# Optimization experiments

Hardware: AMD Instinct MI355X
Metric: run time of the kernel (lower is better)

The kernel has to match this reference:

```python
import jax, jax.numpy as jnp
import numpy as np

B, S, D, H, E = 2, 1024, 1024, 4096, 8


def _xavier(key, shape):
    # matches torch.nn.init.xavier_uniform_ on a 3D tensor: fan_in/out from last two dims
    fan_in, fan_out = shape[-2], shape[-1]
    limit = float(np.sqrt(6.0 / (fan_in + fan_out)))
    return jax.random.uniform(key, shape, jnp.float32, -limit, limit)


def setup_inputs() -> dict:
    key = jax.random.key(0)
    ks = jax.random.split(key, 4)
    x = jax.random.normal(ks[0], (B, S, D), jnp.float32)
    router_w = jax.random.normal(ks[1], (D, E), jnp.float32) * (1.0 / np.sqrt(D))
    router_b = jnp.zeros((E,), jnp.float32)
    fc1_weight = _xavier(ks[2], (E, D, H))
    fc1_bias = jnp.zeros((E, H), jnp.float32)
    fc2_weight = _xavier(ks[3], (E, H, D))
    fc2_bias = jnp.zeros((E, D), jnp.float32)
    return {
        "x": x,
        "router_w": router_w,
        "router_b": router_b,
        "fc1_weight": fc1_weight,
        "fc1_bias": fc1_bias,
        "fc2_weight": fc2_weight,
        "fc2_bias": fc2_bias,
    }


def reference(x, router_w, router_b, fc1_weight, fc1_bias, fc2_weight, fc2_bias):
    b, s, d = x.shape
    x_flat = x.reshape(-1, d)                                  # [T, D]
    logits = x_flat @ router_w + router_b                       # [T, E]
    probs = jax.nn.softmax(logits, axis=-1)                     # [T, E]
    # per-expert FC1 + exact GELU (torch nn.GELU default is erf-based)
    h = jnp.einsum('td,edh->teh', x_flat, fc1_weight) + fc1_bias  # [T, E, H]
    h = jax.nn.gelu(h, approximate=False)
    expert_out = jnp.einsum('teh,ehd->ted', h, fc2_weight) + fc2_bias  # [T, E, D]
    out_flat = jnp.einsum('te,ted->td', probs, expert_out)      # [T, D]
    y = out_flat.reshape(b, s, d)
    router_probs = probs.reshape(b, s, -1)
    return y, router_probs
```

## Files before the change

kernel.cpp:

```cpp
#include <hip/hip_runtime.h>
#include <math.h>


typedef float f32x4 __attribute__((ext_vector_type(4)));
typedef __bf16 bf16x8 __attribute__((ext_vector_type(8)));

#define GLL16(gp, lp)                                                          \
  __builtin_amdgcn_global_load_lds(                                            \
      (const __attribute__((address_space(1))) void*)(gp),                     \
      (__attribute__((address_space(3))) void*)(lp), 16, 0, 0)

__device__ __forceinline__ float gelu_f(float h) {
  return 0.5f * h * (1.f + erff(h * 0.70710678118654752f));
}

__global__ void router_kernel(const float* __restrict__ x,
                              const float* __restrict__ rw,
                              const float* __restrict__ rb,
                              float* __restrict__ P,
                              float* __restrict__ probs_out)
{
  int gid = blockIdx.x * blockDim.x + threadIdx.x;
  int t = gid >> 6;
  int l = gid & 63;
  const float* xr = x + (size_t)t * 1024;
  float a[8];
#pragma unroll
  for (int e = 0; e < 8; ++e) a[e] = 0.f;
  for (int d = l; d < 1024; d += 64) {
    float xv = xr[d];
    f32x4 w0 = *(const f32x4*)(rw + d * 8);
    f32x4 w1 = *(const f32x4*)(rw + d * 8 + 4);
#pragma unroll
    for (int e = 0; e < 4; ++e) a[e] += xv * w0[e];
#pragma unroll
    for (int e = 0; e < 4; ++e) a[4 + e] += xv * w1[e];
  }
#pragma unroll
  for (int off = 32; off > 0; off >>= 1) {
#pragma unroll
    for (int e = 0; e < 8; ++e) a[e] += __shfl_down(a[e], off);
  }
  if (l == 0) {
#pragma unroll
    for (int e = 0; e < 8; ++e) a[e] += rb[e];
    float m = a[0];
#pragma unroll
    for (int e = 1; e < 8; ++e) m = fmaxf(m, a[e]);
    float s = 0.f;
#pragma unroll
    for (int e = 0; e < 8; ++e) { a[e] = __expf(a[e] - m); s += a[e]; }
    float inv = 1.f / s;
#pragma unroll
    for (int e = 0; e < 8; ++e) {
      float p = a[e] * inv;
      if (P) P[t * 8 + e] = p;
      probs_out[t * 8 + e] = p;
    }
  }
}

__global__ void cvt_kernel(const float* __restrict__ src,
                           __bf16* __restrict__ dst)
{
  size_t i = ((size_t)blockIdx.x * 256 + threadIdx.x) * 8;
  f32x4 v0 = *(const f32x4*)(src + i);
  f32x4 v1 = *(const f32x4*)(src + i + 4);
  bf16x8 o;
#pragma unroll
  for (int j = 0; j < 4; ++j) o[j] = (__bf16)v0[j];
#pragma unroll
  for (int j = 0; j < 4; ++j) o[4 + j] = (__bf16)v1[j];
  *(bf16x8*)(dst + i) = o;
}

__global__ void transconv_kernel(const float* __restrict__ src,
                                 __bf16* __restrict__ dst,
                                 int R, int C, int cChunk,
                                 size_t dstLd, size_t zOff)
{
  size_t bs = (size_t)blockIdx.z * (size_t)R * (size_t)C;
  size_t dzo = (size_t)blockIdx.z * zOff;
  int r = blockIdx.x * 256 + threadIdx.x;
  int c0 = blockIdx.y * cChunk;
  const float* s = src + bs + (size_t)r * C;
  for (int c = c0; c < c0 + cChunk; c += 8) {
    f32x4 v0 = *(const f32x4*)(s + c);
    f32x4 v1 = *(const f32x4*)(s + c + 4);
    float vv[8] = {v0[0], v0[1], v0[2], v0[3], v1[0], v1[1], v1[2], v1[3]};
#pragma unroll
    for (int j = 0; j < 8; ++j)
      dst[(size_t)(c + j) * dstLd + dzo + r] = (__bf16)vv[j];
  }
}

__device__ __forceinline__ void mfma_loop(const __bf16* A, const __bf16* B,
                                          int lda, int ldb, int K,
                                          __bf16* As, __bf16* Bs,
                                          f32x4 acc[4][4])
{
  const int tid = threadIdx.x;
  const int w = tid >> 6, l = tid & 63;
  const int rg = l >> 3;
  const int csrc = ((l & 7) ^ rg) << 4;
  const size_t ldaB = (size_t)lda * 2, ldbB = (size_t)ldb * 2;
  const char* Ab = (const char*)A + (size_t)(w * 32 + rg) * ldaB + csrc;
  const char* Bb = (const char*)B + (size_t)(w * 32 + rg) * ldbB + csrc;
  char* AsW = (char*)As + w * 4096;
  char* BsW = (char*)Bs + w * 4096;
  const int wm = w & 1, wn = w >> 1;
  const int m16 = l & 15, quad = l >> 4;
  const int rowA0 = wm * 64 + m16;
  const int rowB0 = wn * 64 + m16;
  const int sw = m16 & 7;

  for (int k0 = 0; k0 < K; k0 += 64) {
    __syncthreads();
    const size_t kB = (size_t)k0 * 2;
#pragma unroll
    for (int i = 0; i < 4; ++i) {
      GLL16(Ab + kB + (size_t)(8 * i) * ldaB, AsW + i * 1024);
      GLL16(Bb + kB + (size_t)(8 * i) * ldbB, BsW + i * 1024);
    }
    __syncthreads();
#pragma unroll
    for (int kk = 0; kk < 2; ++kk) {
      const int pos = ((quad + 4 * kk) ^ sw) << 3;
      bf16x8 af[4], bfr[4];
#pragma unroll
      for (int i = 0; i < 4; ++i)
        af[i] = *(const bf16x8*)(As + (rowA0 + 16 * i) * 64 + pos);
#pragma unroll
      for (int j = 0; j < 4; ++j)
        bfr[j] = *(const bf16x8*)(Bs + (rowB0 + 16 * j) * 64 + pos);
#pragma unroll
      for (int i = 0; i < 4; ++i)
#pragma unroll
        for (int j = 0; j < 4; ++j)
          acc[i][j] = __builtin_amdgcn_mfma_f32_16x16x32_bf16(
              af[i], bfr[j], acc[i][j], 0, 0, 0);
    }
  }
}

__global__ void gemm1_kernel(const __bf16* __restrict__ X,
                             const __bf16* __restrict__ W1T,
                             const float* __restrict__ b1,
                             const float* __restrict__ P,
                             __bf16* __restrict__ Hs,
                             int hs_ld, int e_off, size_t b_zstride)
{
  __shared__ __bf16 As[128 * 64], Bs[128 * 64];
  const int bm = blockIdx.x, bn = blockIdx.y, z = blockIdx.z;
  const int e = z + e_off;
  f32x4 acc[4][4];
  const f32x4 z4 = {0.f, 0.f, 0.f, 0.f};
#pragma unroll
  for (int i = 0; i < 4; ++i)
#pragma unroll
    for (int j = 0; j < 4; ++j) acc[i][j] = z4;

  const __bf16* A = X + (size_t)bm * 128 * 1024;
  const __bf16* B = W1T + (size_t)z * b_zstride + (size_t)bn * 128 * 1024;
  mfma_loop(A, B, 1024, 1024, 1024, As, Bs, acc);

  const int tid = threadIdx.x, w = tid >> 6, l = tid & 63;
  const int wm = w & 1, wn = w >> 1, q = l >> 4, c16 = l & 15;
  const int row0 = bm * 128 + wm * 64 + q * 4;
  const int col0 = bn * 128 + wn * 64 + c16;
  float b1v[4];
#pragma unroll
  for (int j = 0; j < 4; ++j)
    b1v[j] = b1[(size_t)e * 4096 + col0 + j * 16];
  float pv[4][4];
#pragma unroll
  for (int i = 0; i < 4; ++i)
#pragma unroll
    for (int r = 0; r < 4; ++r)
      pv[i][r] = P[(size_t)(row0 + i * 16 + r) * 8 + e];
  const int zcol = (hs_ld == 4096) ? 0 : z * 4096;
#pragma unroll
  for (int i = 0; i < 4; ++i)
#pragma unroll
    for (int j = 0; j < 4; ++j)
#pragma unroll
      for (int r = 0; r < 4; ++r) {
        float h = acc[i][j][r] + b1v[j];
        float o = gelu_f(h) * pv[i][r];
        Hs[(size_t)(row0 + i * 16 + r) * hs_ld + zcol + col0 + j * 16] =
            (__bf16)o;
      }
}

__global__ void gemm2_kernel(const __bf16* __restrict__ Hs,
                             const __bf16* __restrict__ W2T,
                             float* __restrict__ accb,
                             int lda, int ldb, int kz)
{
  __shared__ __bf16 As[128 * 64], Bs[128 * 64];
  const int bm = blockIdx.x, bn = blockIdx.y, z = blockIdx.z;
  f32x4 acc[4][4];
  const f32x4 z4 = {0.f, 0.f, 0.f, 0.f};
#pragma unroll
  for (int i = 0; i < 4; ++i)
#pragma unroll
    for (int j = 0; j < 4; ++j) acc[i][j] = z4;

  const __bf16* A = Hs + (size_t)bm * 128 * lda + (size_t)z * kz;
  const __bf16* B = W2T + (size_t)bn * 128 * ldb + (size_t)z * kz;
  mfma_loop(A, B, lda, ldb, 4096, As, Bs, acc);

  const int tid = threadIdx.x, w = tid >> 6, l = tid & 63;
  const int wm = w & 1, wn = w >> 1, q = l >> 4, c16 = l & 15;
  const int row0 = bm * 128 + wm * 64 + q * 4;
  const int col0 = bn * 128 + wn * 64 + c16;
#pragma unroll
  for (int i = 0; i < 4; ++i)
#pragma unroll
    for (int j = 0; j < 4; ++j)
#pragma unroll
      for (int r = 0; r < 4; ++r)
        unsafeAtomicAdd(
            accb + (size_t)(row0 + i * 16 + r) * 1024 + col0 + j * 16,
            acc[i][j][r]);
}

__global__ void finalize_kernel(const float* __restrict__ accb,
                                const float* __restrict__ P,
                                const float* __restrict__ b2,
                                float* __restrict__ y)
{
  int idx = blockIdx.x * 256 + threadIdx.x;
  int t = idx >> 8;
  int d0 = (idx & 255) << 2;
  f32x4 a = *(const f32x4*)(accb + (size_t)t * 1024 + d0);
#pragma unroll
  for (int e = 0; e < 8; ++e) {
    float p = P[t * 8 + e];
    f32x4 b = *(const f32x4*)(b2 + (size_t)e * 1024 + d0);
#pragma unroll
    for (int c = 0; c < 4; ++c) a[c] += p * b[c];
  }
  *(f32x4*)(y + (size_t)t * 1024 + d0) = a;
}

__global__ __launch_bounds__(256) void fused_naive_kernel(
    const float* __restrict__ x, const float* __restrict__ w1,
    const float* __restrict__ b1, const float* __restrict__ w2,
    const float* __restrict__ b2, const float* __restrict__ probs,
    float* __restrict__ y)
{
  __shared__ float xs[8][1024];
  __shared__ float gs[8][64];
  __shared__ float ps[8];
  const int tid = threadIdx.x;
  const int t0 = blockIdx.x * 8;
  const size_t DH = (size_t)1024 * 4096;
  const int tt = tid >> 5;
  const int d0 = (tid & 31) * 32;
  float acc[32];
#pragma unroll
  for (int i = 0; i < 32; ++i) acc[i] = 0.f;
  {
    const f32x4* xsrc = (const f32x4*)(x + (size_t)t0 * 1024);
    f32x4* xdst = (f32x4*)&xs[0][0];
    for (int i = tid; i < 2048; i += 256) xdst[i] = xsrc[i];
  }
  const int wv = tid >> 6;
  const int hl = tid & 63;
  for (int e = 0; e < 8; ++e) {
    if (tid < 8) ps[tid] = probs[(size_t)(t0 + tid) * 8 + e];
    __syncthreads();
    for (int hc = 0; hc < 4096; hc += 64) {
      float a0 = 0.f, a1 = 0.f;
      const float* w1p = w1 + (size_t)e * DH + hc + hl;
      for (int d = 0; d < 1024; ++d) {
        float wvv = w1p[(size_t)d * 4096];
        a0 += xs[wv * 2 + 0][d] * wvv;
        a1 += xs[wv * 2 + 1][d] * wvv;
      }
      __syncthreads();
      gs[wv * 2 + 0][hl] =
          ps[wv * 2 + 0] * gelu_f(a0 + b1[(size_t)e * 4096 + hc + hl]);
      gs[wv * 2 + 1][hl] =
          ps[wv * 2 + 1] * gelu_f(a1 + b1[(size_t)e * 4096 + hc + hl]);
      __syncthreads();
      const float* w2p = w2 + (size_t)e * DH + (size_t)hc * 1024 + d0;
      for (int hh = 0; hh < 64; ++hh) {
        float g = gs[tt][hh];
#pragma unroll
        for (int jb = 0; jb < 8; ++jb) {
          f32x4 w4 = *(const f32x4*)(w2p + (size_t)hh * 1024 + jb * 4);
#pragma unroll
          for (int j2 = 0; j2 < 4; ++j2) acc[jb * 4 + j2] += g * w4[j2];
        }
      }
    }
#pragma unroll
    for (int j = 0; j < 32; ++j)
      acc[j] += ps[tt] * b2[(size_t)e * 1024 + d0 + j];
    __syncthreads();
  }
  float* yp = y + (size_t)(t0 + tt) * 1024 + d0;
#pragma unroll
  for (int jb = 0; jb < 8; ++jb) {
    f32x4 o = {acc[jb * 4], acc[jb * 4 + 1], acc[jb * 4 + 2], acc[jb * 4 + 3]};
    *(f32x4*)(yp + jb * 4) = o;
  }
}

extern "C" void kernel_launch(void* const* d_in, const int* in_sizes, int n_in,
                              void* d_out, int out_size, void* d_ws,
                              size_t ws_size, hipStream_t stream)
{
  const float* x  = (const float*)d_in[0];
  const float* rw = (const float*)d_in[1];
  const float* rb = (const float*)d_in[2];
  const float* w1 = (const float*)d_in[3];
  const float* b1 = (const float*)d_in[4];
  const float* w2 = (const float*)d_in[5];
  const float* b2 = (const float*)d_in[6];
  float* y = (float*)d_out;
  float* probs_out = y + (size_t)2048 * 1024;

  const size_t DH = (size_t)1024 * 4096;
  const size_t BASE = (64 << 10) + (size_t)2048 * 1024 * 4 +
                      (size_t)2048 * 1024 * 2;
  const size_t TA = BASE + 8 * DH * 2 + (size_t)2048 * 32768 * 2;
  const size_t TB = BASE + DH * 2 + (size_t)2048 * 4096 * 2;

  char* ws = (char*)d_ws;
  float* P = (float*)ws;
  float* accb = (float*)(ws + (64 << 10));
  __bf16* xb = (__bf16*)(ws + (64 << 10) + (size_t)2048 * 1024 * 4);
  char* ws2 = ws + BASE;

  if (ws_size >= TA) {
    router_kernel<<<512, 256, 0, stream>>>(x, rw, rb, P, probs_out);
    hipMemsetAsync(accb, 0, (size_t)2048 * 1024 * 4, stream);
    cvt_kernel<<<1024, 256, 0, stream>>>(x, xb);
    __bf16* WT = (__bf16*)ws2;
    __bf16* Hs = WT + 8 * DH;
    transconv_kernel<<<dim3(4, 64, 8), 256, 0, stream>>>(
        w1, WT, 1024, 4096, 64, 1024, DH);
    gemm1_kernel<<<dim3(16, 32, 8), 256, 0, stream>>>(xb, WT, b1, P, Hs,
                                                      32768, 0, DH);
    transconv_kernel<<<dim3(16, 16, 8), 256, 0, stream>>>(
        w2, WT, 4096, 1024, 64, 32768, 4096);
    gemm2_kernel<<<dim3(16, 8, 8), 256, 0, stream>>>(Hs, WT, accb, 32768,
                                                     32768, 4096);
    finalize_kernel<<<2048, 256, 0, stream>>>(accb, P, b2, y);
  } else if (ws_size >= TB) {
    router_kernel<<<512, 256, 0, stream>>>(x, rw, rb, P, probs_out);
    hipMemsetAsync(accb, 0, (size_t)2048 * 1024 * 4, stream);
    cvt_kernel<<<1024, 256, 0, stream>>>(x, xb);
    __bf16* WT = (__bf16*)ws2;
    __bf16* HsE = WT + DH;
    for (int e = 0; e < 8; ++e) {
      transconv_kernel<<<dim3(4, 64, 1), 256, 0, stream>>>(
          w1 + e * DH, WT, 1024, 4096, 64, 1024, 0);
      gemm1_kernel<<<dim3(16, 32, 1), 256, 0, stream>>>(xb, WT, b1, P, HsE,
                                                        4096, e, 0);
      transconv_kernel<<<dim3(16, 16, 1), 256, 0, stream>>>(
          w2 + e * DH, WT, 4096, 1024, 64, 4096, 0);
      gemm2_kernel<<<dim3(16, 8, 1), 256, 0, stream>>>(HsE, WT, accb, 4096,
                                                       4096, 0);
    }
    finalize_kernel<<<2048, 256, 0, stream>>>(accb, P, b2, y);
  } else {
    router_kernel<<<512, 256, 0, stream>>>(x, rw, rb, (float*)nullptr,
                                           probs_out);
    fused_naive_kernel<<<256, 256, 0, stream>>>(x, w1, b1, w2, b2, probs_out,
                                                y);
  }
}
```

Measured before the change: 712.6 us.

## Use 256x256 tiles with a 4-stage LDS ring and XCD-aware block swizzle

Rewrites the shared MFMA main loop for both expert GEMMs. It now uses 512-thread workgroups computing 256x256 tiles with K-steps of 32 and a 4-deep LDS ring buffer, so global-to-LDS loads run three stages ahead of compute with explicit waitcnt and a single barrier per step. Block IDs are remapped so that neighbouring tiles land on the same XCD for better L2 reuse, and MFMA priority is raised. In exchange it uses 128KB of LDS and many more accumulator registers per workgroup, which limits occupancy. The per-expert fallback path's gemm2 is also split along K across four z slices.

```diff
diff --git a/kernel.cpp b/kernel.cpp
--- a/kernel.cpp
+++ b/kernel.cpp
@@ -94,135 +94,183 @@
   }
 }
 
-__device__ __forceinline__ void mfma_loop(const __bf16* A, const __bf16* B,
-                                          int lda, int ldb, int K,
-                                          __bf16* As, __bf16* Bs,
-                                          f32x4 acc[4][4])
+__device__ __forceinline__ void mfma_loop256(
+    const char* Ab, const char* Bb, size_t ldaB, size_t ldbB, int K,
+    char* lds, f32x4 acc[8][4])
 {
   const int tid = threadIdx.x;
   const int w = tid >> 6, l = tid & 63;
-  const int rg = l >> 3;
-  const int csrc = ((l & 7) ^ rg) << 4;
-  const size_t ldaB = (size_t)lda * 2, ldbB = (size_t)ldb * 2;
-  const char* Ab = (const char*)A + (size_t)(w * 32 + rg) * ldaB + csrc;
-  const char* Bb = (const char*)B + (size_t)(w * 32 + rg) * ldbB + csrc;
-  char* AsW = (char*)As + w * 4096;
-  char* BsW = (char*)Bs + w * 4096;
-  const int wm = w & 1, wn = w >> 1;
-  const int m16 = l & 15, quad = l >> 4;
-  const int rowA0 = wm * 64 + m16;
-  const int rowB0 = wn * 64 + m16;
-  const int sw = m16 & 7;
-
-  for (int k0 = 0; k0 < K; k0 += 64) {
-    __syncthreads();
-    const size_t kB = (size_t)k0 * 2;
-#pragma unroll
-    for (int i = 0; i < 4; ++i) {
-      GLL16(Ab + kB + (size_t)(8 * i) * ldaB, AsW + i * 1024);
-      GLL16(Bb + kB + (size_t)(8 * i) * ldbB, BsW + i * 1024);
-    }
-    __syncthreads();
-#pragma unroll
-    for (int kk = 0; kk < 2; ++kk) {
-      const int pos = ((quad + 4 * kk) ^ sw) << 3;
-      bf16x8 af[4], bfr[4];
-#pragma unroll
-      for (int i = 0; i < 4; ++i)
-        af[i] = *(const bf16x8*)(As + (rowA0 + 16 * i) * 64 + pos);
-#pragma unroll
-      for (int j = 0; j < 4; ++j)
-        bfr[j] = *(const bf16x8*)(Bs + (rowB0 + 16 * j) * 64 + pos);
-#pragma unroll
-      for (int i = 0; i < 4; ++i)
-#pragma unroll
-        for (int j = 0; j < 4; ++j)
-          acc[i][j] = __builtin_amdgcn_mfma_f32_16x16x32_bf16(
-              af[i], bfr[j], acc[i][j], 0, 0, 0);
-    }
-  }
-}
-
-__global__ void gemm1_kernel(const __bf16* __restrict__ X,
-                             const __bf16* __restrict__ W1T,
-                             const float* __restrict__ b1,
-                             const float* __restrict__ P,
-                             __bf16* __restrict__ Hs,
-                             int hs_ld, int e_off, size_t b_zstride)
-{
-  __shared__ __bf16 As[128 * 64], Bs[128 * 64];
-  const int bm = blockIdx.x, bn = blockIdx.y, z = blockIdx.z;
+  const int wm = w >> 2, wn = w & 3;
+  const int m16 = l & 15, q = l >> 4;
+  const int posB = ((q ^ ((m16 >> 1) & 3)) << 4);
+  const int aE = (wm * 128 + m16) * 64 + posB;
+  const int bE = 16384 + (wn * 64 + m16) * 64 + posB;
+  const int sc16 = (((l & 3) ^ ((l >> 3) & 3)) << 4);
+  const size_t sAoff = (size_t)(w * 32 + (l >> 2)) * ldaB + sc16;
+  const size_t sBoff = (size_t)(w * 32 + (l >> 2)) * ldbB + sc16;
+  const int ldst = w * 32 * 64;
+  const int NT = K >> 5;
+
+#define STAGE256(u)                                                            \
+  {                                                                            \
+    char* dA = lds + (((u) & 3) * 32768) + ldst;                               \
+    const char* gA = Ab + sAoff + ((size_t)(u) << 6);                          \
+    GLL16(gA, dA);                                                             \
+    GLL16(gA + 16 * ldaB, dA + 1024);                                          \
+    char* dB = dA + 16384;                                                     \
+    const char* gB = Bb + sBoff + ((size_t)(u) << 6);                          \
+    GLL16(gB, dB);                                                             \
+    GLL16(gB + 16 * ldbB, dB + 1024);                                          \
+  }
+
+#define KFRAGS(T)                                                              \
+    const char* ring = lds + (((T) & 3) * 32768);                              \
+    bf16x8 af[8], bv[4];                                                       \
+    _Pragma("unroll") for (int mi = 0; mi < 8; ++mi)                           \
+        af[mi] = *(const bf16x8*)(ring + aE + mi * 1024);                      \
+    _Pragma("unroll") for (int nj = 0; nj < 4; ++nj)                           \
+        bv[nj] = *(const bf16x8*)(ring + bE + nj * 1024);
+
+#define KMFMA                                                                  \
+    __builtin_amdgcn_sched_barrier(0);                                         \
+    asm volatile("s_waitcnt lgkmcnt(0)" ::: "memory");                         \
+    __builtin_amdgcn_sched_barrier(0);                                         \
+    __builtin_amdgcn_s_setprio(1);                                             \
+    _Pragma("unroll") for (int mi = 0; mi < 8; ++mi)                           \
+      _Pragma("unroll") for (int nj = 0; nj < 4; ++nj)                         \
+        acc[mi][nj] = __builtin_amdgcn_mfma_f32_16x16x32_bf16(                 \
+            af[mi], bv[nj], acc[mi][nj], 0, 0, 0);                             \
+    __builtin_amdgcn_s_setprio(0);                                             \
+    __builtin_amdgcn_sched_barrier(0);
+
+  STAGE256(0);
+  STAGE256(1);
+  STAGE256(2);
+  asm volatile("s_waitcnt vmcnt(8)" ::: "memory");
+  __builtin_amdgcn_s_barrier();
+
+  int t = 0;
+  for (; t < NT - 3; ++t) {
+    KFRAGS(t);
+    STAGE256(t + 3);
+    KMFMA;
+    asm volatile("s_waitcnt vmcnt(8)" ::: "memory");
+    __builtin_amdgcn_s_barrier();
+  }
+  {
+    KFRAGS(t);
+    KMFMA;
+    asm volatile("s_waitcnt vmcnt(0)" ::: "memory");
+    __builtin_amdgcn_s_barrier();
+  }
+  ++t;
+  {
+    KFRAGS(t);
+    KMFMA;
+  }
+  ++t;
+  {
+    KFRAGS(t);
+    KMFMA;
+  }
+#undef STAGE256
+#undef KFRAGS
+#undef KMFMA
+}
+
+__device__ __forceinline__ int xcd_swz(int id, int nwg) {
+  return ((nwg & 7) == 0) ? ((id & 7) * (nwg >> 3) + (id >> 3)) : id;
+}
+
+__global__ __launch_bounds__(512, 2) void gemm1_kernel(
+    const __bf16* __restrict__ X, const __bf16* __restrict__ W1T,
+    const float* __restrict__ b1, const float* __restrict__ P,
+    __bf16* __restrict__ Hs, int hs_ld, int e_off, size_t b_zstride)
+{
+  __shared__ __align__(16) char lds[131072];
+  const int nwg = gridDim.x * gridDim.y * gridDim.z;
+  const int id = blockIdx.x + gridDim.x * (blockIdx.y + gridDim.y * blockIdx.z);
+  const int wg = xcd_swz(id, nwg);
+  const int bm = wg & 7;
+  const int bn = (wg >> 3) % gridDim.y;
+  const int z = wg / (gridDim.y << 3);
   const int e = z + e_off;
-  f32x4 acc[4][4];
+
+  f32x4 acc[8][4];
   const f32x4 z4 = {0.f, 0.f, 0.f, 0.f};
 #pragma unroll
-  for (int i = 0; i < 4; ++i)
+  for (int i = 0; i < 8; ++i)
 #pragma unroll
     for (int j = 0; j < 4; ++j) acc[i][j] = z4;
 
-  const __bf16* A = X + (size_t)bm * 128 * 1024;
-  const __bf16* B = W1T + (size_t)z * b_zstride + (size_t)bn * 128 * 1024;
-  mfma_loop(A, B, 1024, 1024, 1024, As, Bs, acc);
+  const char* A = (const char*)(X + (size_t)bm * 256 * 1024);
+  const char* B = (const char*)(W1T + (size_t)z * b_zstride +
+                                (size_t)bn * 256 * 1024);
+  mfma_loop256(A, B, 2048, 2048, 1024, lds, acc);
 
   const int tid = threadIdx.x, w = tid >> 6, l = tid & 63;
-  const int wm = w & 1, wn = w >> 1, q = l >> 4, c16 = l & 15;
-  const int row0 = bm * 128 + wm * 64 + q * 4;
-  const int col0 = bn * 128 + wn * 64 + c16;
+  const int wm = w >> 2, wn = w & 3, q = l >> 4, m16 = l & 15;
+  const int row0 = bm * 256 + wm * 128 + q * 4;
+  const int colE = bn * 256 + wn * 64 + m16;
+  const int zcol = (hs_ld == 4096) ? 0 : z * 4096;
   float b1v[4];
 #pragma unroll
-  for (int j = 0; j < 4; ++j)
-    b1v[j] = b1[(size_t)e * 4096 + col0 + j * 16];
-  float pv[4][4];
-#pragma unroll
-  for (int i = 0; i < 4; ++i)
+  for (int nj = 0; nj < 4; ++nj)
+    b1v[nj] = b1[(size_t)e * 4096 + colE + nj * 16];
+#pragma unroll
+  for (int mi = 0; mi < 8; ++mi) {
+    float pv[4];
 #pragma unroll
     for (int r = 0; r < 4; ++r)
-      pv[i][r] = P[(size_t)(row0 + i * 16 + r) * 8 + e];
-  const int zcol = (hs_ld == 4096) ? 0 : z * 4096;
-#pragma unroll
-  for (int i = 0; i < 4; ++i)
-#pragma unroll
-    for (int j = 0; j < 4; ++j)
+      pv[r] = P[(size_t)(row0 + mi * 16 + r) * 8 + e];
+#pragma unroll
+    for (int nj = 0; nj < 4; ++nj)
 #pragma unroll
       for (int r = 0; r < 4; ++r) {
-        float h = acc[i][j][r] + b1v[j];
-        float o = gelu_f(h) * pv[i][r];
-        Hs[(size_t)(row0 + i * 16 + r) * hs_ld + zcol + col0 + j * 16] =
+        float h = acc[mi][nj][r] + b1v[nj];
+        float o = gelu_f(h) * pv[r];
+        Hs[(size_t)(row0 + mi * 16 + r) * hs_ld + zcol + colE + nj * 16] =
             (__bf16)o;
       }
-}
-
-__global__ void gemm2_kernel(const __bf16* __restrict__ Hs,
-                             const __bf16* __restrict__ W2T,
-                             float* __restrict__ accb,
-                             int lda, int ldb, int kz)
-{
-  __shared__ __bf16 As[128 * 64], Bs[128 * 64];
-  const int bm = blockIdx.x, bn = blockIdx.y, z = blockIdx.z;
-  f32x4 acc[4][4];
+  }
+}
+
+__global__ __launch_bounds__(512, 2) void gemm2_kernel(
+    const __bf16* __restrict__ Hs, const __bf16* __restrict__ W2T,
+    float* __restrict__ accb, int lda, int ldb, int kz, int Kb)
+{
+  __shared__ __align__(16) char lds[131072];
+  const int nwg = gridDim.x * gridDim.y * gridDim.z;
+  const int id = blockIdx.x + gridDim.x * (blockIdx.y + gridDim.y * blockIdx.z);
+  const int wg = xcd_swz(id, nwg);
+  const int bm = wg & 7;
+  const int bn = (wg >> 3) % gridDim.y;
+  const int z = wg / (gridDim.y << 3);
+
+  f32x4 acc[8][4];
   const f32x4 z4 = {0.f, 0.f, 0.f, 0.f};
 #pragma unroll
-  for (int i = 0; i < 4; ++i)
+  for (int i = 0; i < 8; ++i)
 #pragma unroll
     for (int j = 0; j < 4; ++j) acc[i][j] = z4;
 
-  const __bf16* A = Hs + (size_t)bm * 128 * lda + (size_t)z * kz;
-  const __bf16* B = W2T + (size_t)bn * 128 * ldb + (size_t)z * kz;
-  mfma_loop(A, B, lda, ldb, 4096, As, Bs, acc);
+  const char* A = (const char*)(Hs + (size_t)bm * 256 * lda + (size_t)z * kz);
+  const char* B = (const char*)(W2T + (size_t)bn * 256 * ldb + (size_t)z * kz);
+  mfma_loop256(A, B, (size_t)lda * 2, (size_t)ldb * 2, Kb, lds, acc);
 
   const int tid = threadIdx.x, w = tid >> 6, l = tid & 63;
-  const int wm = w & 1, wn = w >> 1, q = l >> 4, c16 = l & 15;
-  const int row0 = bm * 128 + wm * 64 + q * 4;
-  const int col0 = bn * 128 + wn * 64 + c16;
-#pragma unroll
-  for (int i = 0; i < 4; ++i)
-#pragma unroll
-    for (int j = 0; j < 4; ++j)
+  const int wm = w >> 2, wn = w & 3, q = l >> 4, m16 = l & 15;
+  const int row0 = bm * 256 + wm * 128 + q * 4;
+  const int col0 = bn * 256 + wn * 64 + m16;
+#pragma unroll
+  for (int mi = 0; mi < 8; ++mi)
+#pragma unroll
+    for (int nj = 0; nj < 4; ++nj)
 #pragma unroll
       for (int r = 0; r < 4; ++r)
         unsafeAtomicAdd(
-            accb + (size_t)(row0 + i * 16 + r) * 1024 + col0 + j * 16,
-            acc[i][j][r]);
+            accb + (size_t)(row0 + mi * 16 + r) * 1024 + col0 + nj * 16,
+            acc[mi][nj][r]);
 }
 
 __global__ void finalize_kernel(const float* __restrict__ accb,
@@ -343,12 +391,12 @@
     __bf16* Hs = WT + 8 * DH;
     transconv_kernel<<<dim3(4, 64, 8), 256, 0, stream>>>(
         w1, WT, 1024, 4096, 64, 1024, DH);
-    gemm1_kernel<<<dim3(16, 32, 8), 256, 0, stream>>>(xb, WT, b1, P, Hs,
-                                                      32768, 0, DH);
+    gemm1_kernel<<<dim3(8, 16, 8), 512, 0, stream>>>(xb, WT, b1, P, Hs,
+                                                     32768, 0, DH);
     transconv_kernel<<<dim3(16, 16, 8), 256, 0, stream>>>(
         w2, WT, 4096, 1024, 64, 32768, 4096);
-    gemm2_kernel<<<dim3(16, 8, 8), 256, 0, stream>>>(Hs, WT, accb, 32768,
-                                                     32768, 4096);
+    gemm2_kernel<<<dim3(8, 4, 8), 512, 0, stream>>>(Hs, WT, accb, 32768,
+                                                    32768, 4096, 4096);
     finalize_kernel<<<2048, 256, 0, stream>>>(accb, P, b2, y);
   } else if (ws_size >= TB) {
     router_kernel<<<512, 256, 0, stream>>>(x, rw, rb, P, probs_out);
@@ -359,12 +407,12 @@
     for (int e = 0; e < 8; ++e) {
       transconv_kernel<<<dim3(4, 64, 1), 256, 0, stream>>>(
           w1 + e * DH, WT, 1024, 4096, 64, 1024, 0);
-      gemm1_kernel<<<dim3(16, 32, 1), 256, 0, stream>>>(xb, WT, b1, P, HsE,
-                                                        4096, e, 0);
+      gemm1_kernel<<<dim3(8, 16, 1), 512, 0, stream>>>(xb, WT, b1, P, HsE,
+                                                       4096, e, 0);
       transconv_kernel<<<dim3(16, 16, 1), 256, 0, stream>>>(
           w2 + e * DH, WT, 4096, 1024, 64, 4096, 0);
-      gemm2_kernel<<<dim3(16, 8, 1), 256, 0, stream>>>(HsE, WT, accb, 4096,
-                                                       4096, 0);
+      gemm2_kernel<<<dim3(8, 4, 4), 512, 0, stream>>>(HsE, WT, accb, 4096,
+                                                      4096, 1024, 1024);
     }
     finalize_kernel<<<2048, 256, 0, stream>>>(accb, P, b2, y);
   } else {
```

New measurement: 704.7 us. About the same (-1.1%).
